# Optimization experiments

Hardware: AMD Instinct MI355X
Metric: run time of the kernel (lower is better)

Reference implementation:

```python
import jax, jax.numpy as jnp
import numpy as np

B, S, D = 2, 2048, 2048
H, KVH, HD = 16, 4, 128
ROT = 64  # partial rotary dims (cos/sin last dim = ROT//2)
WINDOW = 1024
EPS = 1e-6


def _rmsnorm(x, scale=None):
    x32 = x.astype(jnp.float32)
    y = x32 * jax.lax.rsqrt(jnp.mean(x32 * x32, axis=-1, keepdims=True) + EPS)
    if scale is not None:
        y = y * (1.0 + scale.astype(jnp.float32))
    return y.astype(x.dtype)


def _rope(x, cos, sin):
    # x: [b, h, s, hd]; rotate first ROT dims, pass through the rest
    x_rot, x_pass = x[..., :ROT], x[..., ROT:]
    x1, x2 = x_rot[..., :ROT // 2], x_rot[..., ROT // 2:]
    rotated = jnp.concatenate([-x2, x1], axis=-1)
    cos_f = jnp.concatenate([cos, cos], axis=-1)[None, None].astype(x.dtype)
    sin_f = jnp.concatenate([sin, sin], axis=-1)[None, None].astype(x.dtype)
    return jnp.concatenate([x_rot * cos_f + rotated * sin_f, x_pass], axis=-1)


def setup_inputs() -> dict:
    key = jax.random.key(0)
    ks = jax.random.split(key, 6)
    x = jax.random.normal(ks[0], (B, S, D), jnp.float32)
    # causal + sliding-window mask (True = masked out)
    i = jnp.arange(S)
    rel = i[:, None] - i[None, :]  # query - key
    mask = (rel < 0) | (rel >= WINDOW)
    # RoPE tables
    inv_freq = 1.0 / (10000.0 ** (jnp.arange(0, ROT, 2, dtype=jnp.float32) / ROT))
    t = jnp.arange(S, dtype=jnp.float32)[:, None] * inv_freq[None, :]  # [S, ROT//2]
    cos, sin = jnp.cos(t), jnp.sin(t)
    init = 0.02
    Wq = jax.random.normal(ks[1], (D, H * HD), jnp.float32) * init
    Wk = jax.random.normal(ks[2], (D, KVH * HD), jnp.float32) * init
    Wv = jax.random.normal(ks[3], (D, KVH * HD), jnp.float32) * init
    Wo = jax.random.normal(ks[4], (H * HD, D), jnp.float32) * init
    q_scale = jnp.zeros((HD,), jnp.float32)  # Gemma RMSNorm weight init = 0, applied as (1+w)
    k_scale = jnp.zeros((HD,), jnp.float32)
    return {"x": x, "mask": mask, "cos": cos, "sin": sin,
            "Wq": Wq, "Wk": Wk, "Wv": Wv, "Wo": Wo,
            "q_scale": q_scale, "k_scale": k_scale}


def reference(x, mask, cos, sin, Wq, Wk, Wv, Wo, q_scale, k_scale):
    b, s, _ = x.shape
    G = H // KVH  # group size
    q = (x @ Wq).reshape(b, s, H, HD).transpose(0, 2, 1, 3)      # [b,H,s,hd]
    q = _rope(_rmsnorm(q, q_scale), cos, sin)
    k = (x @ Wk).reshape(b, s, KVH, HD).transpose(0, 2, 1, 3)    # [b,KVH,s,hd]
    k = _rope(_rmsnorm(k, k_scale), cos, sin)
    v = _rmsnorm((x @ Wv).reshape(b, s, KVH, HD).transpose(0, 2, 1, 3))
    # grouped-head attention (equivalent to repeat_interleave of k/v over groups)
    qg = q.reshape(b, KVH, G, s, HD)
    scores = jnp.einsum('bkgqd,bkld->bkgql', qg, k)              # no 1/sqrt(hd): QK-norm model
    scores = jnp.where(mask[None, None, None], -jnp.inf, scores)
    w = jax.nn.softmax(scores.astype(jnp.float32), axis=-1).astype(q.dtype)
    ctx = jnp.einsum('bkgql,bkld->bkgqd', w, v)                  # [b,KVH,G,s,hd]
    ctx = ctx.reshape(b, H, s, HD).transpose(0, 2, 1, 3).reshape(b, s, H * HD)
    return ctx @ Wo
```

## Files before the change

### kernel.cpp

```cpp
#include <hip/hip_runtime.h>
#include <stdint.h>

#define B_ 2
#define S_ 2048
#define D_ 2048
#define H_ 16
#define KVH_ 4
#define HD_ 128
#define ROT_ 64
#define WINDOW_ 1024
#define EPS_ 1e-6f
#define M_ (B_ * S_)
#define NQKV_ 3072

#define QBLK 128
#define KVBLK 64

typedef unsigned short ushort_t;
typedef _Float16 f16;
typedef float f32x4 __attribute__((ext_vector_type(4)));
typedef f16 f16x8 __attribute__((ext_vector_type(8)));

#define NINF (-__builtin_inff())

__device__ __forceinline__ void gload16(const void* g, void* l) {
  __builtin_amdgcn_global_load_lds(
      (const __attribute__((address_space(1))) void*)g,
      (__attribute__((address_space(3))) void*)l, 16, 0, 0);
}

__launch_bounds__(256, 4)
__global__ void cast_f32_f16(const float* __restrict__ src, f16* __restrict__ dst, int n8) {
  int i = blockIdx.x * 256 + threadIdx.x;
  if (i >= n8) return;
  float4 a = reinterpret_cast<const float4*>(src)[i * 2];
  float4 b = reinterpret_cast<const float4*>(src)[i * 2 + 1];
  f16x8 o = { (f16)a.x, (f16)a.y, (f16)a.z, (f16)a.w,
              (f16)b.x, (f16)b.y, (f16)b.z, (f16)b.w };
  reinterpret_cast<f16x8*>(dst)[i] = o;
}

__launch_bounds__(256, 4)
__global__ void transpose_f32_f16(const float* __restrict__ src, f16* __restrict__ dst,
                                  int R, int C) {
  __shared__ float tile[32][33];
  int c0 = blockIdx.x * 32, r0 = blockIdx.y * 32;
  int tx = threadIdx.x & 31, ty = threadIdx.x >> 5;
#pragma unroll
  for (int i = 0; i < 32; i += 8)
    tile[ty + i][tx] = src[(size_t)(r0 + ty + i) * C + c0 + tx];
  __syncthreads();
#pragma unroll
  for (int i = 0; i < 32; i += 8)
    dst[(size_t)(c0 + ty + i) * R + r0 + tx] = (f16)tile[tx][ty + i];
}

__launch_bounds__(256, 4)
__global__ void transpose16(const ushort_t* __restrict__ src, ushort_t* __restrict__ dst,
                            int R, int C) {
  __shared__ ushort_t tile[32][33];
  size_t base = (size_t)blockIdx.z * R * C;
  src += base; dst += base;
  int c0 = blockIdx.x * 32, r0 = blockIdx.y * 32;
  int tx = threadIdx.x & 31, ty = threadIdx.x >> 5;
#pragma unroll
  for (int i = 0; i < 32; i += 8)
    tile[ty + i][tx] = src[(size_t)(r0 + ty + i) * C + c0 + tx];
  __syncthreads();
#pragma unroll
  for (int i = 0; i < 32; i += 8)
    dst[(size_t)(c0 + ty + i) * R + r0 + tx] = tile[tx][ty + i];
}

__launch_bounds__(256, 2)
__global__ void gemm_f16(const f16* __restrict__ A, const f16* __restrict__ Bt,
                         float* __restrict__ C, int M, int N, int K) {
  __shared__ __attribute__((aligned(16))) f16 As[128][64];
  __shared__ __attribute__((aligned(16))) f16 Bs[128][64];
  const int gx = gridDim.x;
  const int nwg = gx * gridDim.y;
  const int flat = blockIdx.y * gx + blockIdx.x;
  const int q8 = nwg >> 3;
  const int id2 = (flat & 7) * q8 + (flat >> 3);
  const int bm = (id2 / gx) * 128, bn = (id2 % gx) * 128;
  const int tid = threadIdx.x;
  const int lane = tid & 63, wid = tid >> 6;
  const int wm = (wid >> 1) * 64, wn = (wid & 1) * 64;
  const int rr = lane & 15, rg = lane >> 4;
  const int sw = (((lane & 7) ^ (lane >> 3)) << 4);
  const int srw = lane >> 3;
  const char* Ab = (const char*)A + ((size_t)(bm + wid * 32 + srw) * K) * 2 + sw;
  const char* Bb = (const char*)Bt + ((size_t)(bn + wid * 32 + srw) * K) * 2 + sw;
  f32x4 acc[4][4] = {};
  for (int k0 = 0; k0 < K; k0 += 64) {
    __syncthreads();
#pragma unroll
    for (int g = 0; g < 4; ++g) {
      gload16(Ab + (size_t)(g * 8) * K * 2 + (size_t)k0 * 2,
              (char*)&As[0][0] + (wid * 32 + g * 8) * 128);
      gload16(Bb + (size_t)(g * 8) * K * 2 + (size_t)k0 * 2,
              (char*)&Bs[0][0] + (wid * 32 + g * 8) * 128);
    }
    __syncthreads();
    f16x8 af[4][2], bf[4][2];
#pragma unroll
    for (int i = 0; i < 4; ++i)
#pragma unroll
      for (int kk = 0; kk < 2; ++kk) {
        af[i][kk] = *reinterpret_cast<const f16x8*>(
            (const char*)&As[0][0] + (wm + i * 16 + rr) * 128 +
            ((kk * 64 + rg * 16) ^ ((rr & 7) << 4)));
        bf[i][kk] = *reinterpret_cast<const f16x8*>(
            (const char*)&Bs[0][0] + (wn + i * 16 + rr) * 128 +
            ((kk * 64 + rg * 16) ^ ((rr & 7) << 4)));
      }
#pragma unroll
    for (int kk = 0; kk < 2; ++kk)
#pragma unroll
      for (int i = 0; i < 4; ++i)
#pragma unroll
        for (int j = 0; j < 4; ++j)
          acc[i][j] = __builtin_amdgcn_mfma_f32_16x16x32_f16(af[i][kk], bf[j][kk],
                                                             acc[i][j], 0, 0, 0);
  }
#pragma unroll
  for (int i = 0; i < 4; ++i)
#pragma unroll
    for (int j = 0; j < 4; ++j)
#pragma unroll
      for (int r = 0; r < 4; ++r)
        C[(size_t)(bm + wm + i * 16 + rg * 4 + r) * N + (bn + wn + j * 16 + rr)] = acc[i][j][r];
}

__launch_bounds__(256, 4)
__global__ void norm_rope_kv(const float* __restrict__ qkv, const float* __restrict__ cosb,
                             const float* __restrict__ sinb, const float* __restrict__ ksc,
                             f16* __restrict__ kf, f16* __restrict__ vb) {
  int gw = blockIdx.x * 4 + (threadIdx.x >> 6);
  int lane = threadIdx.x & 63;
  int row = gw >> 3, c = gw & 7;
  int b = row >> 11, s = row & (S_ - 1);
  int col = (c < 4) ? (2048 + c * 128) : (2560 + (c - 4) * 128);
  const float* src = qkv + (size_t)row * NQKV_ + col;
  float2 v = *reinterpret_cast<const float2*>(src + lane * 2);
  float ss = v.x * v.x + v.y * v.y;
#pragma unroll
  for (int off = 32; off; off >>= 1) ss += __shfl_xor(ss, off);
  float inv = rsqrtf(ss * (1.0f / HD_) + EPS_);
  float x0 = v.x * inv, x1 = v.y * inv;
  int d0 = lane * 2;
  f16* dst;
  size_t idx;
  if (c < 4) {
    x0 *= (1.0f + ksc[d0]);
    x1 *= (1.0f + ksc[d0 + 1]);
    float y0 = __shfl_xor(x0, 16);
    float y1 = __shfl_xor(x1, 16);
    if (d0 < ROT_) {
      int dm = d0 & 31;
      float cs0 = cosb[s * 32 + dm],     sn0 = sinb[s * 32 + dm];
      float cs1 = cosb[s * 32 + dm + 1], sn1 = sinb[s * 32 + dm + 1];
      if (d0 < 32) { x0 = x0 * cs0 - y0 * sn0; x1 = x1 * cs1 - y1 * sn1; }
      else         { x0 = x0 * cs0 + y0 * sn0; x1 = x1 * cs1 + y1 * sn1; }
    }
    dst = kf; idx = ((size_t)((b * KVH_ + c) * S_ + s)) * HD_ + d0;
  } else {
    dst = vb; idx = ((size_t)((b * KVH_ + (c - 4)) * S_ + s)) * HD_ + d0;
  }
  f16 o[2] = { (f16)x0, (f16)x1 };
  unsigned int pk; __builtin_memcpy(&pk, o, 4);
  *reinterpret_cast<unsigned int*>(dst + idx) = pk;
}

__launch_bounds__(512, 4)
__global__ void flash_attn(const float* __restrict__ qkv, const float* __restrict__ cosb,
                           const float* __restrict__ sinb, const float* __restrict__ qsc,
                           const f16* __restrict__ kfp, const f16* __restrict__ vt,
                           f16* __restrict__ ctxf) {
  __shared__ __attribute__((aligned(16))) f16 Ks[2][KVBLK][128];
  __shared__ __attribute__((aligned(16))) f16 Vs[2][128][KVBLK];
  __shared__ __attribute__((aligned(16))) f16 Pb[8][16][40];
  const int id = blockIdx.x;
  const int g8 = id & 7, wvb = id >> 3;
  const int b = g8 >> 2, kvh = g8 & 3;
  const int h = kvh * 4 + (wvb >> 4);
  const int qtile = wvb & 15;
  const int tid = threadIdx.x;
  const int lane = tid & 63, w = tid >> 6;
  const int rr = lane & 15, rg = lane >> 4;
  const int qBase = qtile * QBLK;
  const int qw = qBase + w * 16;
  const f16* Kh = kfp + (size_t)(b * KVH_ + kvh) * S_ * HD_;
  const f16* Vh = vt  + (size_t)(b * KVH_ + kvh) * HD_ * S_;

  f16x8 qf[4];
  {
    const int srow = qw + rr;
    const float* qrow = qkv + (size_t)(b * S_ + srow) * NQKV_ + h * HD_;
    float qv[4][8];
    float ssq = 0.f;
#pragma unroll
    for (int kk = 0; kk < 4; ++kk) {
      float4 u0 = *reinterpret_cast<const float4*>(qrow + kk * 32 + rg * 8);
      float4 u1 = *reinterpret_cast<const float4*>(qrow + kk * 32 + rg * 8 + 4);
      qv[kk][0] = u0.x; qv[kk][1] = u0.y; qv[kk][2] = u0.z; qv[kk][3] = u0.w;
      qv[kk][4] = u1.x; qv[kk][5] = u1.y; qv[kk][6] = u1.z; qv[kk][7] = u1.w;
#pragma unroll
      for (int j = 0; j < 8; ++j) ssq += qv[kk][j] * qv[kk][j];
    }
    ssq += __shfl_xor(ssq, 16);
    ssq += __shfl_xor(ssq, 32);
    float inv = rsqrtf(ssq * (1.0f / HD_) + EPS_);
#pragma unroll
    for (int kk = 0; kk < 4; ++kk)
#pragma unroll
      for (int j = 0; j < 8; ++j)
        qv[kk][j] *= inv * (1.0f + qsc[kk * 32 + rg * 8 + j]);
    const float* cs = cosb + (size_t)srow * 32;
    const float* sn = sinb + (size_t)srow * 32;
#pragma unroll
    for (int j = 0; j < 8; ++j) {
      int d = rg * 8 + j;
      float c = cs[d], s = sn[d];
      float x0 = qv[0][j], x1 = qv[1][j];
      qv[0][j] = x0 * c - x1 * s;
      qv[1][j] = x1 * c + x0 * s;
    }
#pragma unroll
    for (int kk = 0; kk < 4; ++kk)
#pragma unroll
      for (int j = 0; j < 8; ++j)
        qf[kk][j] = (f16)qv[kk][j];
  }

  f32x4 acc[8] = {};
  f32x4 accl = {};
  float m_run[4];
#pragma unroll
  for (int r = 0; r < 4; ++r) m_run[r] = NINF;
  const f16x8 ones = { (f16)1, (f16)1, (f16)1, (f16)1, (f16)1, (f16)1, (f16)1, (f16)1 };

  int kvStart = qBase - (WINDOW_ - 1);
  if (kvStart < 0) kvStart = 0;
  kvStart &= ~(KVBLK - 1);
  const int ntile = (qBase + QBLK - kvStart) / KVBLK;

  const int k_r0 = lane >> 4;
  const int k_cb = (lane & 15) * 16;
  const int v_r0 = lane >> 3;
  const int v_cb = (lane & 7) * 16;

#define STAGE(bufs, key0_)                                                           \
  do {                                                                               \
    _Pragma("unroll")                                                                \
    for (int gg = 0; gg < 2; ++gg) {                                                 \
      int krow = gg * 4 + k_r0;                                                      \
      gload16((const char*)Kh + (size_t)((key0_) + w * 8 + krow) * 256 +             \
                  (k_cb ^ ((krow & 7) << 4)),                                        \
              (char*)&Ks[bufs][0][0] + (w * 8 + gg * 4) * 256);                      \
      int vrow = gg * 8 + v_r0;                                                      \
      gload16((const char*)Vh + (size_t)(w * 16 + vrow) * (S_ * 2) +                 \
                  (size_t)(key0_) * 2 + (v_cb ^ ((vrow & 7) << 4)),                  \
              (char*)&Vs[bufs][0][0] + (w * 16 + gg * 8) * 128);                     \
    }                                                                                \
  } while (0)

  STAGE(0, kvStart);
  __syncthreads();

  for (int t = 0; t < ntile; ++t) {
    const int key0 = kvStart + t * KVBLK;
    const int buf = t & 1;
    if (t + 1 < ntile) STAGE(buf ^ 1, key0 + KVBLK);

    f32x4 sc[4];
#pragma unroll
    for (int nt = 0; nt < 4; ++nt) {
      const int rt = nt * 16 + rr;
      const char* kbase = (const char*)&Ks[buf][0][0] + rt * 256;
      const int swz = (rt & 7) << 4;
      f32x4 s = {};
#pragma unroll
      for (int kk = 0; kk < 4; ++kk) {
        f16x8 kfr = *reinterpret_cast<const f16x8*>(kbase + ((kk * 64 + rg * 16) ^ swz));
        s = __builtin_amdgcn_mfma_f32_16x16x32_f16(qf[kk], kfr, s, 0, 0, 0);
      }
      sc[nt] = s;
    }

    const bool interior = (key0 + 63 <= qw) && (key0 >= qw - 1008);
    if (!interior) {
#pragma unroll
      for (int nt = 0; nt < 4; ++nt)
#pragma unroll
        for (int r = 0; r < 4; ++r) {
          int qi = qw + rg * 4 + r;
          int kj = key0 + nt * 16 + rr;
          bool valid = (kj <= qi) && (qi - kj < WINDOW_);
          if (!valid) sc[nt][r] = NINF;
        }
    }

    float tmax[4];
#pragma unroll
    for (int r = 0; r < 4; ++r)
      tmax[r] = fmaxf(fmaxf(sc[0][r], sc[1][r]), fmaxf(sc[2][r], sc[3][r]));
#pragma unroll
    for (int off = 1; off < 16; off <<= 1)
#pragma unroll
      for (int r = 0; r < 4; ++r)
        tmax[r] = fmaxf(tmax[r], __shfl_xor(tmax[r], off));

    float alpha[4], msafe[4];
#pragma unroll
    for (int r = 0; r < 4; ++r) {
      float mn = fmaxf(m_run[r], tmax[r]);
      msafe[r] = (mn == NINF) ? 0.f : mn;
      alpha[r] = (m_run[r] == NINF) ? 0.f : __expf(m_run[r] - mn);
      m_run[r] = mn;
    }
#pragma unroll
    for (int nt = 0; nt < 4; ++nt)
#pragma unroll
      for (int r = 0; r < 4; ++r)
        sc[nt][r] = __expf(sc[nt][r] - msafe[r]);
#pragma unroll
    for (int n = 0; n < 8; ++n)
#pragma unroll
      for (int r = 0; r < 4; ++r) acc[n][r] *= alpha[r];
#pragma unroll
    for (int r = 0; r < 4; ++r) accl[r] *= alpha[r];

#pragma unroll
    for (int nt = 0; nt < 2; ++nt)
#pragma unroll
      for (int r = 0; r < 4; ++r)
        Pb[w][rg * 4 + r][nt * 16 + rr] = (f16)sc[nt][r];
    f16x8 pf0 = *reinterpret_cast<const f16x8*>(&Pb[w][rr][rg * 8]);
#pragma unroll
    for (int nt = 0; nt < 2; ++nt)
#pragma unroll
      for (int r = 0; r < 4; ++r)
        Pb[w][rg * 4 + r][nt * 16 + rr] = (f16)sc[2 + nt][r];
    f16x8 pf1 = *reinterpret_cast<const f16x8*>(&Pb[w][rr][rg * 8]);

    __builtin_amdgcn_s_setprio(1);
#pragma unroll
    for (int n = 0; n < 8; ++n) {
      const int d = n * 16 + rr;
      const char* vbase = (const char*)&Vs[buf][0][0] + d * 128;
      const int swz = (d & 7) << 4;
      f16x8 vf0 = *reinterpret_cast<const f16x8*>(vbase + ((rg * 16) ^ swz));
      f16x8 vf1 = *reinterpret_cast<const f16x8*>(vbase + ((64 + rg * 16) ^ swz));
      acc[n] = __builtin_amdgcn_mfma_f32_16x16x32_f16(pf0, vf0, acc[n], 0, 0, 0);
      acc[n] = __builtin_amdgcn_mfma_f32_16x16x32_f16(pf1, vf1, acc[n], 0, 0, 0);
    }
    accl = __builtin_amdgcn_mfma_f32_16x16x32_f16(pf0, ones, accl, 0, 0, 0);
    accl = __builtin_amdgcn_mfma_f32_16x16x32_f16(pf1, ones, accl, 0, 0, 0);
    __builtin_amdgcn_s_setprio(0);

    __syncthreads();
  }
#undef STAGE

#pragma unroll
  for (int n = 0; n < 8; ++n)
#pragma unroll
    for (int r = 0; r < 4; ++r) {
      float o = acc[n][r] / accl[r];
      int qi = qw + rg * 4 + r;
      ctxf[(size_t)(b * S_ + qi) * D_ + h * HD_ + n * 16 + rr] = (f16)o;
    }
}

extern "C" void kernel_launch(void* const* d_in, const int* in_sizes, int n_in,
                              void* d_out, int out_size, void* d_ws, size_t ws_size,
                              hipStream_t stream) {
  const float* x    = (const float*)d_in[0];
  const float* cosb = (const float*)d_in[2];
  const float* sinb = (const float*)d_in[3];
  const float* Wq   = (const float*)d_in[4];
  const float* Wk   = (const float*)d_in[5];
  const float* Wv   = (const float*)d_in[6];
  const float* Wo   = (const float*)d_in[7];
  const float* qsc  = (const float*)d_in[8];
  const float* ksc  = (const float*)d_in[9];
  float* out = (float*)d_out;

  char* ws = (char*)d_ws;
  const size_t MB = 1ull << 20;
  f16* xh    = (f16*)(ws + 0 * MB);
  f16* ctxf  = (f16*)(ws + 0 * MB);
  f16* wqkvT = (f16*)(ws + 16 * MB);
  f16* kf    = (f16*)(ws + 16 * MB);
  f16* vb    = (f16*)(ws + 20 * MB);
  f16* vtb   = (f16*)(ws + 24 * MB);
  f16* woT   = (f16*)(ws + 28 * MB);
  float* qkv = (float*)(ws + 36 * MB);

  cast_f32_f16<<<dim3(M_ * D_ / 8 / 256), 256, 0, stream>>>(x, xh, M_ * D_ / 8);
  transpose_f32_f16<<<dim3(64, 64), 256, 0, stream>>>(Wq, wqkvT, D_, 2048);
  transpose_f32_f16<<<dim3(16, 64), 256, 0, stream>>>(Wk, wqkvT + (size_t)2048 * D_, D_, 512);
  transpose_f32_f16<<<dim3(16, 64), 256, 0, stream>>>(Wv, wqkvT + (size_t)2560 * D_, D_, 512);
  transpose_f32_f16<<<dim3(64, 64), 256, 0, stream>>>(Wo, woT, D_, D_);
  gemm_f16<<<dim3(NQKV_ / 128, M_ / 128), 256, 0, stream>>>(xh, wqkvT, qkv, M_, NQKV_, D_);
  norm_rope_kv<<<dim3(M_ * 8 / 4), 256, 0, stream>>>(qkv, cosb, sinb, ksc, kf, vb);
  transpose16<<<dim3(HD_ / 32, S_ / 32, B_ * KVH_), 256, 0, stream>>>(
      (const ushort_t*)vb, (ushort_t*)vtb, S_, HD_);
  flash_attn<<<dim3((S_ / QBLK) * H_ * B_), 512, 0, stream>>>(
      qkv, cosb, sinb, qsc, kf, vtb, ctxf);
  gemm_f16<<<dim3(D_ / 128, M_ / 128), 256, 0, stream>>>(ctxf, woT, out, M_, D_, D_);
}
```

Before: 219.5 us.

## Double-buffer GEMM tiles, use exp2 softmax with lazy rescale, reorder attention tiles

The GEMM now double-buffers its LDS tiles, so the next K-slice load is issued before the MFMAs on the current one, with one barrier per iteration instead of two. The attention softmax folds log2(e) into K so it can use exp2, and it skips rescaling the accumulator when the running max grows by at most 8 (base-2 units). The block-to-tile mapping is reordered so the later, longer query tiles are scheduled first, which should balance load. The costs are extra shared memory in the GEMM, which may lower occupancy, and some headroom in fp16 P values from the deferred rescale.

```diff
diff --git a/kernel.cpp b/kernel.cpp
--- a/kernel.cpp
+++ b/kernel.cpp
@@ -15,6 +15,8 @@
 
 #define QBLK 128
 #define KVBLK 64
+#define LOG2E 1.44269504088896340736f
+#define DEFER_THR 8.0f
 
 typedef unsigned short ushort_t;
 typedef _Float16 f16;
@@ -22,6 +24,7 @@
 typedef f16 f16x8 __attribute__((ext_vector_type(8)));
 
 #define NINF (-__builtin_inff())
+#define EXP2F(x) __builtin_exp2f(x)
 
 __device__ __forceinline__ void gload16(const void* g, void* l) {
   __builtin_amdgcn_global_load_lds(
@@ -75,8 +78,8 @@
 __launch_bounds__(256, 2)
 __global__ void gemm_f16(const f16* __restrict__ A, const f16* __restrict__ Bt,
                          float* __restrict__ C, int M, int N, int K) {
-  __shared__ __attribute__((aligned(16))) f16 As[128][64];
-  __shared__ __attribute__((aligned(16))) f16 Bs[128][64];
+  __shared__ __attribute__((aligned(16))) f16 As[2][128][64];
+  __shared__ __attribute__((aligned(16))) f16 Bs[2][128][64];
   const int gx = gridDim.x;
   const int nwg = gx * gridDim.y;
   const int flat = blockIdx.y * gx + blockIdx.x;
@@ -92,26 +95,34 @@
   const char* Ab = (const char*)A + ((size_t)(bm + wid * 32 + srw) * K) * 2 + sw;
   const char* Bb = (const char*)Bt + ((size_t)(bn + wid * 32 + srw) * K) * 2 + sw;
   f32x4 acc[4][4] = {};
-  for (int k0 = 0; k0 < K; k0 += 64) {
-    __syncthreads();
-#pragma unroll
-    for (int g = 0; g < 4; ++g) {
-      gload16(Ab + (size_t)(g * 8) * K * 2 + (size_t)k0 * 2,
-              (char*)&As[0][0] + (wid * 32 + g * 8) * 128);
-      gload16(Bb + (size_t)(g * 8) * K * 2 + (size_t)k0 * 2,
-              (char*)&Bs[0][0] + (wid * 32 + g * 8) * 128);
-    }
-    __syncthreads();
+
+#define STAGEG(bf, k0_)                                                          \
+  do {                                                                           \
+    _Pragma("unroll")                                                            \
+    for (int g = 0; g < 4; ++g) {                                                \
+      gload16(Ab + (size_t)(g * 8) * K * 2 + (size_t)(k0_) * 2,                  \
+              (char*)&As[bf][0][0] + (wid * 32 + g * 8) * 128);                  \
+      gload16(Bb + (size_t)(g * 8) * K * 2 + (size_t)(k0_) * 2,                  \
+              (char*)&Bs[bf][0][0] + (wid * 32 + g * 8) * 128);                  \
+    }                                                                            \
+  } while (0)
+
+  const int ntk = K >> 6;
+  STAGEG(0, 0);
+  __syncthreads();
+  int buf = 0;
+  for (int t = 0; t < ntk; ++t) {
+    if (t + 1 < ntk) STAGEG(buf ^ 1, (t + 1) * 64);
     f16x8 af[4][2], bf[4][2];
 #pragma unroll
     for (int i = 0; i < 4; ++i)
 #pragma unroll
       for (int kk = 0; kk < 2; ++kk) {
         af[i][kk] = *reinterpret_cast<const f16x8*>(
-            (const char*)&As[0][0] + (wm + i * 16 + rr) * 128 +
+            (const char*)&As[buf][0][0] + (wm + i * 16 + rr) * 128 +
             ((kk * 64 + rg * 16) ^ ((rr & 7) << 4)));
         bf[i][kk] = *reinterpret_cast<const f16x8*>(
-            (const char*)&Bs[0][0] + (wn + i * 16 + rr) * 128 +
+            (const char*)&Bs[buf][0][0] + (wn + i * 16 + rr) * 128 +
             ((kk * 64 + rg * 16) ^ ((rr & 7) << 4)));
       }
 #pragma unroll
@@ -122,7 +133,10 @@
         for (int j = 0; j < 4; ++j)
           acc[i][j] = __builtin_amdgcn_mfma_f32_16x16x32_f16(af[i][kk], bf[j][kk],
                                                              acc[i][j], 0, 0, 0);
+    __syncthreads();
+    buf ^= 1;
   }
+#undef STAGEG
 #pragma unroll
   for (int i = 0; i < 4; ++i)
 #pragma unroll
@@ -163,6 +177,7 @@
       if (d0 < 32) { x0 = x0 * cs0 - y0 * sn0; x1 = x1 * cs1 - y1 * sn1; }
       else         { x0 = x0 * cs0 + y0 * sn0; x1 = x1 * cs1 + y1 * sn1; }
     }
+    x0 *= LOG2E; x1 *= LOG2E;
     dst = kf; idx = ((size_t)((b * KVH_ + c) * S_ + s)) * HD_ + d0;
   } else {
     dst = vb; idx = ((size_t)((b * KVH_ + (c - 4)) * S_ + s)) * HD_ + d0;
@@ -183,8 +198,10 @@
   const int id = blockIdx.x;
   const int g8 = id & 7, wvb = id >> 3;
   const int b = g8 >> 2, kvh = g8 & 3;
-  const int h = kvh * 4 + (wvb >> 4);
-  const int qtile = wvb & 15;
+  int hh, qtile;
+  if (wvb < 32) { hh = wvb >> 3; qtile = 8 + (wvb & 7); }
+  else { int lv = wvb - 32; hh = lv >> 3; qtile = lv & 7; }
+  const int h = kvh * 4 + hh;
   const int tid = threadIdx.x;
   const int lane = tid & 63, w = tid >> 6;
   const int rr = lane & 15, rg = lane >> 4;
@@ -235,9 +252,9 @@
 
   f32x4 acc[8] = {};
   f32x4 accl = {};
-  float m_run[4];
-#pragma unroll
-  for (int r = 0; r < 4; ++r) m_run[r] = NINF;
+  float m_run[4], msafe[4];
+#pragma unroll
+  for (int r = 0; r < 4; ++r) { m_run[r] = NINF; msafe[r] = 0.f; }
   const f16x8 ones = { (f16)1, (f16)1, (f16)1, (f16)1, (f16)1, (f16)1, (f16)1, (f16)1 };
 
   int kvStart = qBase - (WINDOW_ - 1);
@@ -311,25 +328,31 @@
       for (int r = 0; r < 4; ++r)
         tmax[r] = fmaxf(tmax[r], __shfl_xor(tmax[r], off));
 
-    float alpha[4], msafe[4];
-#pragma unroll
-    for (int r = 0; r < 4; ++r) {
-      float mn = fmaxf(m_run[r], tmax[r]);
-      msafe[r] = (mn == NINF) ? 0.f : mn;
-      alpha[r] = (m_run[r] == NINF) ? 0.f : __expf(m_run[r] - mn);
-      m_run[r] = mn;
+    bool defer = true;
+#pragma unroll
+    for (int r = 0; r < 4; ++r)
+      defer = defer && (tmax[r] - m_run[r] <= DEFER_THR);
+    if (!__all(defer)) {
+      float alpha[4];
+#pragma unroll
+      for (int r = 0; r < 4; ++r) {
+        float mn = fmaxf(m_run[r], tmax[r]);
+        alpha[r] = (m_run[r] == NINF) ? 0.f : EXP2F(m_run[r] - mn);
+        m_run[r] = mn;
+        msafe[r] = (mn == NINF) ? 0.f : mn;
+      }
+#pragma unroll
+      for (int n = 0; n < 8; ++n)
+#pragma unroll
+        for (int r = 0; r < 4; ++r) acc[n][r] *= alpha[r];
+#pragma unroll
+      for (int r = 0; r < 4; ++r) accl[r] *= alpha[r];
     }
 #pragma unroll
     for (int nt = 0; nt < 4; ++nt)
 #pragma unroll
       for (int r = 0; r < 4; ++r)
-        sc[nt][r] = __expf(sc[nt][r] - msafe[r]);
-#pragma unroll
-    for (int n = 0; n < 8; ++n)
-#pragma unroll
-      for (int r = 0; r < 4; ++r) acc[n][r] *= alpha[r];
-#pragma unroll
-    for (int r = 0; r < 4; ++r) accl[r] *= alpha[r];
+        sc[nt][r] = EXP2F(sc[nt][r] - msafe[r]);
 
 #pragma unroll
     for (int nt = 0; nt < 2; ++nt)
```

After: 224.8 us. +2.4%, slower.
